# Performance work log

Measured on AMD Instinct MI355X. Metric: run time of the kernel, lower is better.

Reference implementation:

```python
import jax, jax.numpy as jnp
import numpy as np

B, SC, ST = 16, 512, 512
DP, DC = 256, 128
D = DP + 2 * DC          # 512 = d_model
H, L, DFF = 8, 2, 2048
NCAT, NCONT = 1000, 2048


def sin_embed(vals, d, scale=1000.0):
    # vectorized sinusoidal_time_embedding: even dims -> sin(angle), odd dims -> cos(angle)
    i = jnp.arange(d, dtype=jnp.float32)
    ang = vals.astype(jnp.float32)[..., None] / jnp.power(scale, i / d)
    return jnp.where(i % 2 == 0, jnp.sin(ang), jnp.cos(ang))


def layer_norm(x, g, b, eps=1e-5):
    m = jnp.mean(x, -1, keepdims=True)
    v = jnp.mean(jnp.square(x - m), -1, keepdims=True)
    return (x - m) / jnp.sqrt(v + eps) * g + b


def setup_inputs() -> dict:
    key = jax.random.key(0)
    ks = jax.random.split(key, 16)
    s = 0.02
    def n(k, shape, scale=s):
        return jax.random.normal(k, shape, dtype=jnp.float32) * scale
    return {
        "context_cat": jax.random.randint(ks[0], (B, SC), 0, NCAT),
        "context_time": jax.random.uniform(ks[1], (B, SC), dtype=jnp.float32) * 100.0,
        "context_f0": jax.random.uniform(ks[2], (B, SC), dtype=jnp.float32) * 500.0,
        "target_cat": jax.random.randint(ks[3], (B, ST), 0, NCAT),
        "target_time": jax.random.uniform(ks[4], (B, ST), dtype=jnp.float32) * 100.0,
        "target_f0": jax.random.uniform(ks[5], (B, ST), dtype=jnp.float32) * 500.0,
        "cat_table": n(ks[6], (NCAT, DP), 1.0),
        "cont_table": sin_embed(jnp.arange(NCONT, dtype=jnp.float32), DC),  # frozen sin table
        "pad_emb": n(ks[7], (D,), 1.0),
        "Wq": n(ks[8], (L, D, D)), "bq": jnp.zeros((L, D)),
        "Wk": n(ks[9], (L, D, D)), "bk": jnp.zeros((L, D)),
        "Wv": n(ks[10], (L, D, D)), "bv": jnp.zeros((L, D)),
        "Wo": n(ks[11], (L, D, D)), "bo": jnp.zeros((L, D)),
        "ln1g": jnp.ones((L, D)), "ln1b": jnp.zeros((L, D)),
        "ln2g": jnp.ones((L, D)), "ln2b": jnp.zeros((L, D)),
        "W1": n(ks[12], (L, D, DFF)), "b1": jnp.zeros((L, DFF)),
        "W2": n(ks[13], (L, DFF, D)), "b2": jnp.zeros((L, D)),
    }


def reference(context_cat, context_time, context_f0, target_cat, target_time, target_f0,
              cat_table, cont_table, pad_emb,
              Wq, bq, Wk, bk, Wv, bv, Wo, bo,
              ln1g, ln1b, ln2g, ln2b, W1, b1, W2, b2):
    def embed(cat, tm, f0):
        pad = cat < 0
        e = jnp.concatenate(
            [cat_table[jnp.maximum(cat, 0)], sin_embed(tm, DC), sin_embed(f0, DC)], axis=-1)
        return jnp.where(pad[..., None], pad_emb, e), pad

    ce, cp = embed(context_cat, context_time, context_f0)
    te, tp = embed(target_cat, target_time, target_f0)
    x = jnp.concatenate([ce, te], axis=1)                       # [B, SC+ST, D]
    bias = jnp.where(jnp.concatenate([cp, tp], 1), -1e9, 0.0)[:, None, None, :]
    hd = D // H
    inv_sqrt = 1.0 / np.sqrt(hd).astype(np.float32)

    def step(h, p):
        wq, bq_, wk, bk_, wv, bv_, wo, bo_, g1, c1, g2, c2, w1, d1, w2, d2 = p
        Bn, S, _ = h.shape
        q = (h @ wq + bq_).reshape(Bn, S, H, hd)
        k = (h @ wk + bk_).reshape(Bn, S, H, hd)
        v = (h @ wv + bv_).reshape(Bn, S, H, hd)
        scores = jnp.einsum('bqhd,bkhd->bhqk', q, k) * inv_sqrt + bias
        attn = jax.nn.softmax(scores, axis=-1)
        o = jnp.einsum('bhqk,bkhd->bqhd', attn, v).reshape(Bn, S, D)
        h = layer_norm(h + o @ wo + bo_, g1, c1)                # post-norm (torch default)
        f = jax.nn.relu(h @ w1 + d1) @ w2 + d2
        return layer_norm(h + f, g2, c2), None

    x, _ = jax.lax.scan(step, x, (Wq, bq, Wk, bk, Wv, bv, Wo, bo,
                                  ln1g, ln1b, ln2g, ln2b, W1, b1, W2, b2))
    out = x[:, SC:, :]
    pred_cat = out[..., :DP] @ cat_table.T
    pred_time = out[..., DP:DP + DC] @ cont_table.T
    pred_f0 = out[..., DP + DC:] @ cont_table.T
    return pred_cat, pred_time, pred_f0
```

## Files before the change

### kernel.cpp

```cpp
#include <hip/hip_runtime.h>


typedef _Float16 half8 __attribute__((ext_vector_type(8)));
typedef _Float16 half4 __attribute__((ext_vector_type(4)));
typedef float f32x4 __attribute__((ext_vector_type(4)));

__device__ __forceinline__ void gl2lds16(const _Float16* g, _Float16* l) {
    __builtin_amdgcn_global_load_lds(
        (const __attribute__((address_space(1))) void*)g,
        (__attribute__((address_space(3))) void*)l, 16, 0, 0);
}

__global__ void cast_f32_f16_k(const float* __restrict__ in, _Float16* __restrict__ out,
                               long nsrc, long ntot) {
    long i = (long)blockIdx.x * blockDim.x + threadIdx.x;
    long stride = (long)gridDim.x * blockDim.x;
    for (; i < ntot; i += stride) out[i] = i < nsrc ? (_Float16)in[i] : (_Float16)0.f;
}

__global__ void tcast_k(const float* __restrict__ in, _Float16* __restrict__ out,
                        int R, int C, long zs, int rowoff) {
    __shared__ float tile[32][33];
    long z = blockIdx.z;
    const float* src = in + z * (long)R * C;
    _Float16* dst = out + z * zs + (long)rowoff * R;
    int c0 = blockIdx.x * 32, r0 = blockIdx.y * 32;
    for (int i = threadIdx.y; i < 32; i += 8)
        tile[i][threadIdx.x] = src[(long)(r0 + i) * C + c0 + threadIdx.x];
    __syncthreads();
    for (int i = threadIdx.y; i < 32; i += 8)
        dst[(long)(c0 + i) * R + r0 + threadIdx.x] = (_Float16)tile[threadIdx.x][i];
}

__global__ void bcat_k(const float* __restrict__ bq, const float* __restrict__ bk,
                       const float* __restrict__ bv, float* __restrict__ out, int L) {
    int i = blockIdx.x * 256 + threadIdx.x;
    if (i >= L * 1536) return;
    int l = i / 1536, j = i - l * 1536;
    float v = j < 512 ? bq[l * 512 + j] : (j < 1024 ? bk[l * 512 + j - 512] : bv[l * 512 + j - 1024]);
    out[i] = v;
}

__global__ void vtrans_k(const _Float16* __restrict__ qkv, _Float16* __restrict__ vT) {
    __shared__ _Float16 tile[32][33];
    int bh = blockIdx.z; int b = bh >> 3, h = bh & 7;
    int s0 = blockIdx.x * 32, d0 = blockIdx.y * 32;
    const _Float16* src = qkv + ((long)b * 1024) * 1536 + 1024 + h * 64;
    _Float16* dst = vT + (long)bh * 64 * 1024;
    for (int i = threadIdx.y; i < 32; i += 8)
        tile[i][threadIdx.x] = src[(long)(s0 + i) * 1536 + d0 + threadIdx.x];
    __syncthreads();
    for (int i = threadIdx.y; i < 32; i += 8)
        dst[(long)(d0 + i) * 1024 + s0 + threadIdx.x] = tile[threadIdx.x][i];
}

__global__ __launch_bounds__(128) void embed_k(
    const int* __restrict__ ccat, const float* __restrict__ ctime, const float* __restrict__ cf0,
    const int* __restrict__ tcat, const float* __restrict__ ttime, const float* __restrict__ tf0,
    const float* __restrict__ cat_table, const float* __restrict__ pad_emb,
    float* __restrict__ xf, _Float16* __restrict__ xb, float* __restrict__ biasKey) {
    int t = blockIdx.x;
    int b = t >> 10, s = t & 1023;
    int j = b * 512 + (s & 511);
    int cat; float tm, f0;
    if (s < 512) { cat = ccat[j]; tm = ctime[j]; f0 = cf0[j]; }
    else         { cat = tcat[j]; tm = ttime[j]; f0 = tf0[j]; }
    bool pad = cat < 0;
    if (threadIdx.x == 0) biasKey[t] = pad ? -1e9f : 0.f;
    int c = cat < 0 ? 0 : cat;
    #pragma unroll
    for (int u = 0; u < 4; u++) {
        int d = threadIdx.x * 4 + u;
        float val;
        if (pad) val = pad_emb[d];
        else if (d < 256) val = cat_table[(long)c * 256 + d];
        else {
            float base = (d < 384) ? tm : f0;
            int i = (d < 384) ? (d - 256) : (d - 384);
            float ang = base / powf(1000.f, (float)i * (1.f / 128.f));
            val = (i & 1) ? cosf(ang) : sinf(ang);
        }
        long o = (long)t * 512 + d;
        xf[o] = val;
        xb[o] = (_Float16)val;
    }
}

__global__ __launch_bounds__(256) void layernorm_k(
    float* xf, _Float16* __restrict__ xb,
    const float* __restrict__ g, const float* __restrict__ beta) {
    long row = blockIdx.x;
    int tid = threadIdx.x;
    float* xr = xf + row * 512;
    float v0 = xr[tid], v1 = xr[tid + 256];
    float s = v0 + v1, q = v0 * v0 + v1 * v1;
    #pragma unroll
    for (int o = 32; o; o >>= 1) { s += __shfl_down(s, o); q += __shfl_down(q, o); }
    __shared__ float rs[4], rq[4];
    if ((tid & 63) == 0) { rs[tid >> 6] = s; rq[tid >> 6] = q; }
    __syncthreads();
    s = rs[0] + rs[1] + rs[2] + rs[3];
    q = rq[0] + rq[1] + rq[2] + rq[3];
    float mean = s * (1.f / 512.f);
    float var = q * (1.f / 512.f) - mean * mean;
    float rstd = rsqrtf(var + 1e-5f);
    float y0 = (v0 - mean) * rstd * g[tid] + beta[tid];
    float y1 = (v1 - mean) * rstd * g[tid + 256] + beta[tid + 256];
    xr[tid] = y0; xr[tid + 256] = y1;
    xb[row * 512 + tid] = (_Float16)y0;
    xb[row * 512 + tid + 256] = (_Float16)y1;
}

__global__ __launch_bounds__(256) void flash_k(
    const _Float16* __restrict__ QKV, const _Float16* __restrict__ VT,
    const float* __restrict__ biasKey, _Float16* __restrict__ O) {
    const int S = 1024, D = 512, LDQ = 1536;
    int bh = blockIdx.x; int b = bh >> 3, h = bh & 7;
    int qt = blockIdx.y;
    int tid = threadIdx.x, w = tid >> 6, lane = tid & 63;
    int g = lane >> 4, q15 = lane & 15;

    __shared__ __align__(16) _Float16 Ks[128][72];
    __shared__ __align__(16) _Float16 VTs[64][136];
    __shared__ __align__(16) _Float16 Ps[4][16][136];
    __shared__ __align__(16) float biasLds[1024];

    {
        const float* bsrc = biasKey + (long)b * S;
        *(f32x4*)&biasLds[tid * 4] = *(const f32x4*)&bsrc[tid * 4];
    }

    int qrow = qt * 64 + w * 16 + q15;
    const _Float16* qp = QKV + ((long)(b * S + qrow)) * LDQ + h * 64 + g * 8;
    half8 qf[2];
    qf[0] = *(const half8*)(qp);
    qf[1] = *(const half8*)(qp + 32);

    f32x4 acc_o[4];
    #pragma unroll
    for (int i = 0; i < 4; i++)
        #pragma unroll
        for (int r = 0; r < 4; r++) acc_o[i][r] = 0.f;
    float m_run = -1e30f, l_run = 0.f;

    const _Float16* kbase = QKV + 512 + ((long)b * S) * LDQ + h * 64;
    const _Float16* vbase = VT + (long)bh * 64 * S;

    for (int kt = 0; kt < 8; kt++) {
        __syncthreads();
        #pragma unroll
        for (int i = 0; i < 4; i++) {
            int c = tid + i * 256;
            int row = c >> 3, cc = c & 7;
            uint4 v = *(const uint4*)(kbase + (long)(kt * 128 + row) * LDQ + cc * 8);
            *(uint4*)&Ks[row][cc * 8] = v;
        }
        #pragma unroll
        for (int i = 0; i < 4; i++) {
            int c = tid + i * 256;
            int row = c >> 4, cc = c & 15;
            uint4 v = *(const uint4*)(vbase + (long)row * S + kt * 128 + cc * 8);
            *(uint4*)&VTs[row][cc * 8] = v;
        }
        __syncthreads();

        f32x4 acc[8];
        #pragma unroll
        for (int mf = 0; mf < 8; mf++)
            #pragma unroll
            for (int r = 0; r < 4; r++) acc[mf][r] = 0.f;
        #pragma unroll
        for (int kk = 0; kk < 2; kk++)
            #pragma unroll
            for (int mf = 0; mf < 8; mf++) {
                half8 kf = *(const half8*)&Ks[mf * 16 + q15][kk * 32 + g * 8];
                acc[mf] = __builtin_amdgcn_mfma_f32_16x16x32_f16(kf, qf[kk], acc[mf], 0, 0, 0);
            }

        float mt = -1e30f;
        #pragma unroll
        for (int mf = 0; mf < 8; mf++) {
            f32x4 b4 = *(const f32x4*)&biasLds[kt * 128 + mf * 16 + g * 4];
            #pragma unroll
            for (int r = 0; r < 4; r++) {
                float sv = acc[mf][r] * 0.125f + b4[r];
                acc[mf][r] = sv;
                mt = fmaxf(mt, sv);
            }
        }
        mt = fmaxf(mt, __shfl_xor(mt, 16));
        mt = fmaxf(mt, __shfl_xor(mt, 32));
        float m_new = fmaxf(m_run, mt);
        float scale = __expf(m_run - m_new);
        float rsum = 0.f;
        #pragma unroll
        for (int mf = 0; mf < 8; mf++)
            #pragma unroll
            for (int r = 0; r < 4; r++) {
                float p = __expf(acc[mf][r] - m_new);
                acc[mf][r] = p;
                rsum += p;
            }
        rsum += __shfl_xor(rsum, 16);
        rsum += __shfl_xor(rsum, 32);
        l_run = l_run * scale + rsum;
        m_run = m_new;

        float sc[4];
        #pragma unroll
        for (int r = 0; r < 4; r++) sc[r] = __shfl(scale, g * 4 + r);
        #pragma unroll
        for (int nf = 0; nf < 4; nf++)
            #pragma unroll
            for (int r = 0; r < 4; r++) acc_o[nf][r] *= sc[r];

        #pragma unroll
        for (int mf = 0; mf < 8; mf++) {
            half4 h4;
            #pragma unroll
            for (int r = 0; r < 4; r++) h4[r] = (_Float16)acc[mf][r];
            *(half4*)&Ps[w][q15][mf * 16 + g * 4] = h4;
        }

        #pragma unroll
        for (int kk = 0; kk < 4; kk++) {
            half8 pa = *(const half8*)&Ps[w][q15][kk * 32 + g * 8];
            #pragma unroll
            for (int nf = 0; nf < 4; nf++) {
                half8 vf = *(const half8*)&VTs[nf * 16 + q15][kk * 32 + g * 8];
                acc_o[nf] = __builtin_amdgcn_mfma_f32_16x16x32_f16(pa, vf, acc_o[nf], 0, 0, 0);
            }
        }
    }

    float linv = 1.f / l_run;
    float lv[4];
    #pragma unroll
    for (int r = 0; r < 4; r++) lv[r] = __shfl(linv, g * 4 + r);
    _Float16* obase = O + ((long)(b * S + qt * 64 + w * 16)) * D + h * 64;
    #pragma unroll
    for (int nf = 0; nf < 4; nf++)
        #pragma unroll
        for (int r = 0; r < 4; r++) {
            int row = g * 4 + r;
            obase[(long)row * D + nf * 16 + q15] = (_Float16)(acc_o[nf][r] * lv[r]);
        }
}

__global__ __launch_bounds__(256) void gemm_nt(
    const _Float16* __restrict__ A, long lda, long sA1, long sA2,
    const _Float16* __restrict__ Bm, long ldb, long sB1, long sB2,
    float* Cf, _Float16* Cb, long ldc, long sC1, long sC2,
    const float* __restrict__ bias, long sb1, long sb2,
    const float* resid,
    int M, int N, int K, int Z2, float alpha, int relu) {
    int z = blockIdx.z;
    int z1 = z / Z2, z2 = z - z1 * Z2;
    A  += z1 * sA1 + z2 * sA2;
    Bm += z1 * sB1 + z2 * sB2;
    long coff = z1 * sC1 + z2 * sC2;
    if (bias) bias += z1 * sb1 + z2 * sb2;

    int gx = gridDim.x;
    int nwg = gx * gridDim.y;
    int bid = blockIdx.y * gx + blockIdx.x;
    int q = nwg >> 3, r = nwg & 7;
    int xcd = bid & 7, ii = bid >> 3;
    int swz = (xcd < r ? xcd * (q + 1) : r * (q + 1) + (xcd - r) * q) + ii;
    int m0 = (swz / gx) * 128;
    int n0 = (swz % gx) * 128;

    __shared__ __align__(16) _Float16 As[2][128 * 32];
    __shared__ __align__(16) _Float16 Bs[2][128 * 32];

    int tid = threadIdx.x;
    int lane = tid & 63;
    int w = tid >> 6;
    int wr = (w >> 1) << 6;
    int wc = (w & 1) << 6;

    f32x4 acc[4][4];
    #pragma unroll
    for (int i = 0; i < 4; i++)
        #pragma unroll
        for (int jj = 0; jj < 4; jj++) { acc[i][jj][0] = 0.f; acc[i][jj][1] = 0.f; acc[i][jj][2] = 0.f; acc[i][jj][3] = 0.f; }

    int fr = lane & 15;
    int g = lane >> 4;
    int rs8 = (g ^ (fr & 3)) * 8;

    auto stage = [&](int buf, int kt) {
        #pragma unroll
        for (int i = 0; i < 2; i++) {
            int idx = tid + i * 256;
            int row = idx >> 2, s = idx & 3;
            int sg = s ^ (row & 3);
            gl2lds16(A + (long)(m0 + row) * lda + kt * 32 + sg * 8, &As[buf][idx * 8]);
            gl2lds16(Bm + (long)(n0 + row) * ldb + kt * 32 + sg * 8, &Bs[buf][idx * 8]);
        }
    };

    int nk = K >> 5;
    stage(0, 0);
    __syncthreads();

    int cur = 0;
    for (int kt = 0; kt < nk; kt++) {
        if (kt + 1 < nk) stage(cur ^ 1, kt + 1);
        half8 af[4], bfv[4];
        #pragma unroll
        for (int m = 0; m < 4; m++) af[m] = *(const half8*)&As[cur][(wr + m * 16 + fr) * 32 + rs8];
        #pragma unroll
        for (int n = 0; n < 4; n++) bfv[n] = *(const half8*)&Bs[cur][(wc + n * 16 + fr) * 32 + rs8];
        #pragma unroll
        for (int m = 0; m < 4; m++)
            #pragma unroll
            for (int n = 0; n < 4; n++)
                acc[m][n] = __builtin_amdgcn_mfma_f32_16x16x32_f16(af[m], bfv[n], acc[m][n], 0, 0, 0);
        __syncthreads();
        cur ^= 1;
    }

    int fq = lane >> 4;
    #pragma unroll
    for (int m = 0; m < 4; m++) {
        #pragma unroll
        for (int jj = 0; jj < 4; jj++) {
            long row = m0 + wr + m * 16 + fq * 4 + jj;
            #pragma unroll
            for (int n = 0; n < 4; n++) {
                int col = n0 + wc + n * 16 + fr;
                if (col < N) {
                    float v = acc[m][n][jj] * alpha;
                    if (bias) v += bias[col];
                    long o = coff + row * ldc + col;
                    if (resid) v += resid[o];
                    if (relu) v = fmaxf(v, 0.f);
                    if (Cf) Cf[o] = v;
                    if (Cb) Cb[o] = (_Float16)v;
                }
            }
        }
    }
}

extern "C" void kernel_launch(void* const* d_in, const int* in_sizes, int n_in,
                              void* d_out, int out_size, void* d_ws, size_t ws_size,
                              hipStream_t stream) {
    const int Bn = 16, S = 1024, D = 512, H = 8, L = 2, DFF = 2048, NCAT = 1000, NCONT = 2048;
    const long M = (long)Bn * S;

    const int*   ccat      = (const int*)d_in[0];
    const float* ctime     = (const float*)d_in[1];
    const float* cf0       = (const float*)d_in[2];
    const int*   tcat      = (const int*)d_in[3];
    const float* ttime     = (const float*)d_in[4];
    const float* tf0       = (const float*)d_in[5];
    const float* cat_table = (const float*)d_in[6];
    const float* cont_tab  = (const float*)d_in[7];
    const float* pad_emb   = (const float*)d_in[8];
    const float* Wq = (const float*)d_in[9];
    const float* bq = (const float*)d_in[10];
    const float* Wk = (const float*)d_in[11];
    const float* bk = (const float*)d_in[12];
    const float* Wv = (const float*)d_in[13];
    const float* bv = (const float*)d_in[14];
    const float* Wo = (const float*)d_in[15];
    const float* bo = (const float*)d_in[16];
    const float* ln1g = (const float*)d_in[17];
    const float* ln1b = (const float*)d_in[18];
    const float* ln2g = (const float*)d_in[19];
    const float* ln2b = (const float*)d_in[20];
    const float* W1 = (const float*)d_in[21];
    const float* b1 = (const float*)d_in[22];
    const float* W2 = (const float*)d_in[23];
    const float* b2 = (const float*)d_in[24];

    char* wsb = (char*)d_ws;
    size_t off = 0;
    auto alloc = [&](size_t bytes) -> void* {
        off = (off + 255) & ~(size_t)255;
        void* p = wsb + off; off += bytes; return p;
    };

    float*     xf      = (float*)alloc(M * D * 4);
    _Float16*  xb      = (_Float16*)alloc(M * D * 2);
    _Float16*  qkv     = (_Float16*)alloc(M * 3 * D * 2);
    _Float16*  vT      = (_Float16*)alloc(M * D * 2);
    _Float16*  ob      = (_Float16*)alloc(M * D * 2);
    float*     biasKey = (float*)alloc(M * 4);
    _Float16*  WqkvT = (_Float16*)alloc((size_t)L * 3 * D * D * 2);
    float*     bqkv  = (float*)alloc((size_t)L * 3 * D * 4);
    _Float16*  WoT  = (_Float16*)alloc((size_t)L * D * D * 2);
    _Float16*  W1T  = (_Float16*)alloc((size_t)L * D * DFF * 2);
    _Float16*  W2T  = (_Float16*)alloc((size_t)L * DFF * D * 2);
    _Float16*  catT = (_Float16*)alloc((size_t)1024 * 256 * 2);
    _Float16*  conT = (_Float16*)alloc((size_t)NCONT * 128 * 2);

    size_t need_ffh = (size_t)M * DFF * 2;
    _Float16* ffh;
    size_t offAl = (off + 255) & ~(size_t)255;
    if (offAl + need_ffh <= ws_size) ffh = (_Float16*)alloc(need_ffh);
    else ffh = (_Float16*)d_out;

    auto gemm = [&](const _Float16* A, long lda, long sA1, long sA2,
                    const _Float16* Bm, long ldb, long sB1, long sB2,
                    float* Cf, _Float16* Cb, long ldc, long sC1, long sC2,
                    const float* bias, long sb1, long sb2,
                    const float* resid, int Mm, int Nn, int Kk,
                    int Z1, int Z2, float alpha, int relu) {
        dim3 gdim((Nn + 127) / 128, (Mm + 127) / 128, Z1 * Z2);
        gemm_nt<<<gdim, 256, 0, stream>>>(A, lda, sA1, sA2, Bm, ldb, sB1, sB2,
                                          Cf, Cb, ldc, sC1, sC2, bias, sb1, sb2,
                                          resid, Mm, Nn, Kk, Z2, alpha, relu);
    };

    dim3 tb(32, 8);
    tcast_k<<<dim3(D / 32, D / 32, L), tb, 0, stream>>>(Wq, WqkvT, D, D, (long)3 * D * D, 0);
    tcast_k<<<dim3(D / 32, D / 32, L), tb, 0, stream>>>(Wk, WqkvT, D, D, (long)3 * D * D, D);
    tcast_k<<<dim3(D / 32, D / 32, L), tb, 0, stream>>>(Wv, WqkvT, D, D, (long)3 * D * D, 2 * D);
    bcat_k<<<dim3((L * 1536 + 255) / 256), 256, 0, stream>>>(bq, bk, bv, bqkv, L);
    tcast_k<<<dim3(D / 32, D / 32, L), tb, 0, stream>>>(Wo, WoT, D, D, (long)D * D, 0);
    tcast_k<<<dim3(DFF / 32, D / 32, L), tb, 0, stream>>>(W1, W1T, D, DFF, (long)D * DFF, 0);
    tcast_k<<<dim3(D / 32, DFF / 32, L), tb, 0, stream>>>(W2, W2T, DFF, D, (long)DFF * D, 0);
    cast_f32_f16_k<<<dim3(512), 256, 0, stream>>>(cat_table, catT, (long)NCAT * 256, (long)1024 * 256);
    cast_f32_f16_k<<<dim3(512), 256, 0, stream>>>(cont_tab, conT, (long)NCONT * 128, (long)NCONT * 128);

    embed_k<<<dim3((unsigned)M), 128, 0, stream>>>(ccat, ctime, cf0, tcat, ttime, tf0,
                                                   cat_table, pad_emb, xf, xb, biasKey);

    for (int l = 0; l < L; l++) {
        gemm(xb, D, 0, 0, WqkvT + (size_t)l * 3 * D * D, D, 0, 0, nullptr, qkv, 3 * D, 0, 0,
             bqkv + (size_t)l * 3 * D, 0, 0, nullptr, (int)M, 3 * D, D, 1, 1, 1.f, 0);
        vtrans_k<<<dim3(32, 2, Bn * H), tb, 0, stream>>>(qkv, vT);

        flash_k<<<dim3(Bn * H, S / 64), 256, 0, stream>>>(qkv, vT, biasKey, ob);

        gemm(ob, D, 0, 0, WoT + (size_t)l * D * D, D, 0, 0, xf, nullptr, D, 0, 0,
             bo + l * D, 0, 0, xf, (int)M, D, D, 1, 1, 1.f, 0);
        layernorm_k<<<dim3((unsigned)M), 256, 0, stream>>>(xf, xb, ln1g + l * D, ln1b + l * D);

        gemm(xb, D, 0, 0, W1T + (size_t)l * D * DFF, D, 0, 0, nullptr, ffh, DFF, 0, 0,
             b1 + l * DFF, 0, 0, nullptr, (int)M, DFF, D, 1, 1, 1.f, 1);
        gemm(ffh, DFF, 0, 0, W2T + (size_t)l * DFF * D, DFF, 0, 0, xf, nullptr, D, 0, 0,
             b2 + l * D, 0, 0, xf, (int)M, D, DFF, 1, 1, 1.f, 0);
        layernorm_k<<<dim3((unsigned)M), 256, 0, stream>>>(xf, xb, ln2g + l * D, ln2b + l * D);
    }

    float* out_cat  = (float*)d_out;
    float* out_time = out_cat + (size_t)Bn * 512 * NCAT;
    float* out_f0   = out_time + (size_t)Bn * 512 * NCONT;
    gemm(xb + (size_t)512 * D, D, (long)S * D, 0,
         catT, 256, 0, 0,
         out_cat, nullptr, NCAT, (long)512 * NCAT, 0,
         nullptr, 0, 0, nullptr, 512, NCAT, 256, Bn, 1, 1.f, 0);
    gemm(xb + (size_t)512 * D + 256, D, (long)S * D, 0,
         conT, 128, 0, 0,
         out_time, nullptr, NCONT, (long)512 * NCONT, 0,
         nullptr, 0, 0, nullptr, 512, NCONT, 128, Bn, 1, 1.f, 0);
    gemm(xb + (size_t)512 * D + 384, D, (long)S * D, 0,
         conT, 128, 0, 0,
         out_f0, nullptr, NCONT, (long)512 * NCONT, 0,
         nullptr, 0, 0, nullptr, 512, NCONT, 128, Bn, 1, 1.f, 0);
}
```

Baseline: 926.7 us.

## Double-buffer flash attention K/V tiles with async LDS loads and lazy rescale

Reworks the flash attention kernel to use 64-key tiles double-buffered in LDS, filled by direct global-to-LDS loads with an XOR swizzle so the next tile loads while the current one computes. The softmax scale and log2e are folded into Q and the bias so exp2 can be used. Rescaling of the running max is skipped when the new max grows by no more than 8. MFMA priority hints and an occupancy launch bound are added. The per-tile loop is now twice as long with a single barrier, and the loop trades occupancy and register pressure against overlap. Q is pre-scaled in fp16, which slightly changes rounding.

```diff
diff --git a/kernel.cpp b/kernel.cpp
--- a/kernel.cpp
+++ b/kernel.cpp
@@ -111,23 +111,26 @@
     xb[row * 512 + tid + 256] = (_Float16)y1;
 }
 
-__global__ __launch_bounds__(256) void flash_k(
+__global__ __launch_bounds__(256, 3) void flash_k(
     const _Float16* __restrict__ QKV, const _Float16* __restrict__ VT,
     const float* __restrict__ biasKey, _Float16* __restrict__ O) {
-    const int S = 1024, D = 512, LDQ = 1536;
+    const int S = 1024, D = 512, LDQ = 1536, NT = 16;
     int bh = blockIdx.x; int b = bh >> 3, h = bh & 7;
     int qt = blockIdx.y;
     int tid = threadIdx.x, w = tid >> 6, lane = tid & 63;
     int g = lane >> 4, q15 = lane & 15;
 
-    __shared__ __align__(16) _Float16 Ks[128][72];
-    __shared__ __align__(16) _Float16 VTs[64][136];
-    __shared__ __align__(16) _Float16 Ps[4][16][136];
+    __shared__ __align__(16) _Float16 Ks[2][64 * 64];
+    __shared__ __align__(16) _Float16 VTs[2][64 * 64];
+    __shared__ __align__(16) _Float16 Ps[4][16][72];
     __shared__ __align__(16) float biasLds[1024];
 
     {
         const float* bsrc = biasKey + (long)b * S;
-        *(f32x4*)&biasLds[tid * 4] = *(const f32x4*)&bsrc[tid * 4];
+        f32x4 bv4 = *(const f32x4*)&bsrc[tid * 4];
+        #pragma unroll
+        for (int r = 0; r < 4; r++) bv4[r] *= 1.442695041f;
+        *(f32x4*)&biasLds[tid * 4] = bv4;
     }
 
     int qrow = qt * 64 + w * 16 + q15;
@@ -135,6 +138,25 @@
     half8 qf[2];
     qf[0] = *(const half8*)(qp);
     qf[1] = *(const half8*)(qp + 32);
+    const _Float16 qsc = (_Float16)0.1803368801f;
+    #pragma unroll
+    for (int kk = 0; kk < 2; kk++)
+        #pragma unroll
+        for (int i = 0; i < 8; i++) qf[kk][i] *= qsc;
+
+    const _Float16* kbase = QKV + 512 + ((long)b * S) * LDQ + h * 64;
+    const _Float16* vbase = VT + (long)bh * 64 * S;
+
+    auto stage = [&](int buf, int kt) {
+        #pragma unroll
+        for (int i = 0; i < 2; i++) {
+            int c = tid + i * 256;
+            int row = c >> 3, p = c & 7;
+            int s = p ^ (row & 7);
+            gl2lds16(kbase + (long)(kt * 64 + row) * LDQ + s * 8, &Ks[buf][c * 8]);
+            gl2lds16(vbase + (long)row * S + kt * 64 + s * 8, &VTs[buf][c * 8]);
+        }
+    };
 
     f32x4 acc_o[4];
     #pragma unroll
@@ -143,94 +165,96 @@
         for (int r = 0; r < 4; r++) acc_o[i][r] = 0.f;
     float m_run = -1e30f, l_run = 0.f;
 
-    const _Float16* kbase = QKV + 512 + ((long)b * S) * LDQ + h * 64;
-    const _Float16* vbase = VT + (long)bh * 64 * S;
-
-    for (int kt = 0; kt < 8; kt++) {
+    stage(0, 0);
+    int cur = 0;
+    for (int kt = 0; kt < NT; kt++) {
         __syncthreads();
-        #pragma unroll
-        for (int i = 0; i < 4; i++) {
-            int c = tid + i * 256;
-            int row = c >> 3, cc = c & 7;
-            uint4 v = *(const uint4*)(kbase + (long)(kt * 128 + row) * LDQ + cc * 8);
-            *(uint4*)&Ks[row][cc * 8] = v;
-        }
-        #pragma unroll
-        for (int i = 0; i < 4; i++) {
-            int c = tid + i * 256;
-            int row = c >> 4, cc = c & 15;
-            uint4 v = *(const uint4*)(vbase + (long)row * S + kt * 128 + cc * 8);
-            *(uint4*)&VTs[row][cc * 8] = v;
-        }
-        __syncthreads();
-
-        f32x4 acc[8];
-        #pragma unroll
-        for (int mf = 0; mf < 8; mf++)
+        if (kt + 1 < NT) stage(cur ^ 1, kt + 1);
+
+        f32x4 acc[4];
+        #pragma unroll
+        for (int mf = 0; mf < 4; mf++)
             #pragma unroll
             for (int r = 0; r < 4; r++) acc[mf][r] = 0.f;
+        __builtin_amdgcn_s_setprio(1);
         #pragma unroll
         for (int kk = 0; kk < 2; kk++)
             #pragma unroll
-            for (int mf = 0; mf < 8; mf++) {
-                half8 kf = *(const half8*)&Ks[mf * 16 + q15][kk * 32 + g * 8];
+            for (int mf = 0; mf < 4; mf++) {
+                int row = mf * 16 + q15;
+                half8 kf = *(const half8*)&Ks[cur][row * 64 + (((kk * 4 + g) ^ (row & 7)) * 8)];
                 acc[mf] = __builtin_amdgcn_mfma_f32_16x16x32_f16(kf, qf[kk], acc[mf], 0, 0, 0);
             }
+        __builtin_amdgcn_s_setprio(0);
 
         float mt = -1e30f;
         #pragma unroll
-        for (int mf = 0; mf < 8; mf++) {
-            f32x4 b4 = *(const f32x4*)&biasLds[kt * 128 + mf * 16 + g * 4];
+        for (int mf = 0; mf < 4; mf++) {
+            f32x4 b4 = *(const f32x4*)&biasLds[kt * 64 + mf * 16 + g * 4];
             #pragma unroll
             for (int r = 0; r < 4; r++) {
-                float sv = acc[mf][r] * 0.125f + b4[r];
+                float sv = acc[mf][r] + b4[r];
                 acc[mf][r] = sv;
                 mt = fmaxf(mt, sv);
             }
         }
         mt = fmaxf(mt, __shfl_xor(mt, 16));
         mt = fmaxf(mt, __shfl_xor(mt, 32));
-        float m_new = fmaxf(m_run, mt);
-        float scale = __expf(m_run - m_new);
+
         float rsum = 0.f;
-        #pragma unroll
-        for (int mf = 0; mf < 8; mf++)
-            #pragma unroll
-            for (int r = 0; r < 4; r++) {
-                float p = __expf(acc[mf][r] - m_new);
-                acc[mf][r] = p;
-                rsum += p;
-            }
+        if (__all((int)(mt - m_run <= 8.f))) {
+            #pragma unroll
+            for (int mf = 0; mf < 4; mf++)
+                #pragma unroll
+                for (int r = 0; r < 4; r++) {
+                    float p = exp2f(acc[mf][r] - m_run);
+                    acc[mf][r] = p; rsum += p;
+                }
+        } else {
+            float m_new = fmaxf(m_run, mt);
+            float scale = exp2f(m_run - m_new);
+            #pragma unroll
+            for (int mf = 0; mf < 4; mf++)
+                #pragma unroll
+                for (int r = 0; r < 4; r++) {
+                    float p = exp2f(acc[mf][r] - m_new);
+                    acc[mf][r] = p; rsum += p;
+                }
+            float sc[4];
+            #pragma unroll
+            for (int r = 0; r < 4; r++) sc[r] = __shfl(scale, g * 4 + r);
+            #pragma unroll
+            for (int nf = 0; nf < 4; nf++)
+                #pragma unroll
+                for (int r = 0; r < 4; r++) acc_o[nf][r] *= sc[r];
+            l_run *= scale;
+            m_run = m_new;
+        }
         rsum += __shfl_xor(rsum, 16);
         rsum += __shfl_xor(rsum, 32);
-        l_run = l_run * scale + rsum;
-        m_run = m_new;
-
-        float sc[4];
-        #pragma unroll
-        for (int r = 0; r < 4; r++) sc[r] = __shfl(scale, g * 4 + r);
-        #pragma unroll
-        for (int nf = 0; nf < 4; nf++)
-            #pragma unroll
-            for (int r = 0; r < 4; r++) acc_o[nf][r] *= sc[r];
-
-        #pragma unroll
-        for (int mf = 0; mf < 8; mf++) {
+        l_run += rsum;
+
+        #pragma unroll
+        for (int mf = 0; mf < 4; mf++) {
             half4 h4;
             #pragma unroll
             for (int r = 0; r < 4; r++) h4[r] = (_Float16)acc[mf][r];
             *(half4*)&Ps[w][q15][mf * 16 + g * 4] = h4;
         }
 
-        #pragma unroll
-        for (int kk = 0; kk < 4; kk++) {
+        __builtin_amdgcn_s_setprio(1);
+        #pragma unroll
+        for (int kk = 0; kk < 2; kk++) {
             half8 pa = *(const half8*)&Ps[w][q15][kk * 32 + g * 8];
             #pragma unroll
             for (int nf = 0; nf < 4; nf++) {
-                half8 vf = *(const half8*)&VTs[nf * 16 + q15][kk * 32 + g * 8];
+                int row = nf * 16 + q15;
+                half8 vf = *(const half8*)&VTs[cur][row * 64 + (((kk * 4 + g) ^ (row & 7)) * 8)];
                 acc_o[nf] = __builtin_amdgcn_mfma_f32_16x16x32_f16(pa, vf, acc_o[nf], 0, 0, 0);
             }
         }
+        __builtin_amdgcn_s_setprio(0);
+        cur ^= 1;
     }
 
     float linv = 1.f / l_run;
```

New measurement: 921.1 us. Within noise of the previous version (-0.6%).
